# Kernel tuning notes

Hardware: AMD Instinct MI355X
Metric: run time of the kernel (lower is better)

The kernel has to match this reference:

```python
import jax, jax.numpy as jnp
import numpy as np

N_HEADS = 16
D_HEAD = 64
QUERY_DIM = 1024
CONTEXT_DIM = 1024
INNER = N_HEADS * D_HEAD


def setup_inputs() -> dict:
    key = jax.random.key(0)
    ks = jax.random.split(key, 7)
    B, Nq, Nk = 4, 1024, 1024
    x = jax.random.normal(ks[0], (B, Nq, QUERY_DIM), dtype=jnp.float32)
    context = jax.random.normal(ks[1], (B, Nk, CONTEXT_DIM), dtype=jnp.float32)
    s_q = 1.0 / np.sqrt(QUERY_DIM)
    s_c = 1.0 / np.sqrt(CONTEXT_DIM)
    s_i = 1.0 / np.sqrt(INNER)
    Wq = jax.random.uniform(ks[2], (QUERY_DIM, INNER), jnp.float32, -s_q, s_q)
    Wk = jax.random.uniform(ks[3], (CONTEXT_DIM, INNER), jnp.float32, -s_c, s_c)
    Wv = jax.random.uniform(ks[4], (CONTEXT_DIM, INNER), jnp.float32, -s_c, s_c)
    Wo = jax.random.uniform(ks[5], (INNER, QUERY_DIM), jnp.float32, -s_i, s_i)
    bo = jax.random.uniform(ks[6], (QUERY_DIM,), jnp.float32, -s_i, s_i)
    return {"x": x, "context": context, "Wq": Wq, "Wk": Wk, "Wv": Wv, "Wo": Wo, "bo": bo}


def reference(x, context, Wq, Wk, Wv, Wo, bo):
    B, Nq, _ = x.shape
    Nk = context.shape[1]
    scale = D_HEAD ** -0.5
    # project and split heads: [B, H, N, d]
    q = (x @ Wq).reshape(B, Nq, N_HEADS, D_HEAD).transpose(0, 2, 1, 3)
    k = (context @ Wk).reshape(B, Nk, N_HEADS, D_HEAD).transpose(0, 2, 1, 3)
    v = (context @ Wv).reshape(B, Nk, N_HEADS, D_HEAD).transpose(0, 2, 1, 3)
    scores = jnp.einsum("bhqd,bhkd->bhqk", q, k) * scale
    attn = jax.nn.softmax(scores, axis=-1)
    out = jnp.einsum("bhqk,bhkd->bhqd", attn, v)
    out = out.transpose(0, 2, 1, 3).reshape(B, Nq, INNER)
    return out @ Wo + bo
```

## Files before the change

### kernel.cpp

```cpp
#include <hip/hip_runtime.h>
#include <hip/hip_bf16.h>

#define BATCH 4
#define NQ 1024
#define NKK 1024
#define HD 1024
#define NHEADS 16

typedef __bf16 bf16x8 __attribute__((ext_vector_type(8)));
typedef float f32x4 __attribute__((ext_vector_type(4)));
typedef unsigned short u16;
typedef unsigned int u32;

__device__ __forceinline__ u16 f2bf(float f) {
    union { __bf16 h; u16 u; } v;
    v.h = (__bf16)f;
    return v.u;
}

#define GLOAD16(gp, lp) \
    __builtin_amdgcn_global_load_lds((const __attribute__((address_space(1))) void*)(gp), \
                                     (__attribute__((address_space(3))) void*)(lp), 16, 0, 0)

#define MFMA16(a, b, c) __builtin_amdgcn_mfma_f32_16x16x32_bf16(a, b, c, 0, 0, 0)

__global__ __launch_bounds__(256) void cvt2bf_k(const float* __restrict__ a,
                                                u16* __restrict__ o, int n4) {
    int i = blockIdx.x * blockDim.x + threadIdx.x;
    const int stride = gridDim.x * blockDim.x;
    for (; i < n4; i += stride) {
        float4 v = ((const float4*)a)[i];
        ushort4 p;
        p.x = f2bf(v.x); p.y = f2bf(v.y); p.z = f2bf(v.z); p.w = f2bf(v.w);
        ((ushort4*)o)[i] = p;
    }
}

__global__ __launch_bounds__(256) void transpose4_k(const float* __restrict__ w0,
                                                    const float* __restrict__ w1,
                                                    const float* __restrict__ w2,
                                                    const float* __restrict__ w3,
                                                    u16* __restrict__ ws) {
    const float* src = blockIdx.z == 0 ? w0 : blockIdx.z == 1 ? w1 : blockIdx.z == 2 ? w2 : w3;
    const float scl = (blockIdx.z == 0) ? 0.18033688011112042f : 1.0f;
    u16* dst = ws + (size_t)blockIdx.z * (1024u * 1024u);
    __shared__ u16 t[64][65];
    const int bx = blockIdx.x * 64;
    const int by = blockIdx.y * 64;
    const int tid = threadIdx.x;
#pragma unroll
    for (int p = 0; p < 16; ++p) {
        int idx = p * 256 + tid;
        int r = idx >> 6, c = idx & 63;
        t[c][r] = f2bf(scl * src[(size_t)(by + r) * 1024 + bx + c]);
    }
    __syncthreads();
#pragma unroll
    for (int p = 0; p < 16; ++p) {
        int idx = p * 256 + tid;
        int r = idx >> 6, c = idx & 63;
        dst[(size_t)(bx + r) * 1024 + by + c] = t[r][c];
    }
}

__global__ __launch_bounds__(512) void gemm_qkv(const u16* __restrict__ Xb,
                                                const u16* __restrict__ Cb,
                                                const u16* __restrict__ WqT,
                                                const u16* __restrict__ WkT,
                                                const u16* __restrict__ WvT,
                                                u16* __restrict__ Qb,
                                                u16* __restrict__ Kb,
                                                u16* __restrict__ VTb) {
    const int bid = blockIdx.x;
    const int swz = (bid & 7) * 96 + (bid >> 3);
    const int z = swz >> 8;
    const int rem = swz & 255;
    const int m0 = (rem >> 3) * 128;
    const int n0 = (rem & 7) * 128;

    const u16* __restrict__ A  = (z == 0) ? Xb : Cb;
    const u16* __restrict__ BT = (z == 0) ? WqT : (z == 1) ? WkT : WvT;

    __shared__ __align__(16) u16 Asm[128 * 64];
    __shared__ __align__(16) u16 Bsm[128 * 64];

    const int tid = threadIdx.x, lane = tid & 63, wv = tid >> 6;
    const int wm = wv >> 2, wn = wv & 3;
    const int lr = lane & 15, lg = lane >> 4;
    const int lx = lr & 7;
    const int M = BATCH * NQ, N = HD, K = HD;

    f32x4 acc[4][2];
#pragma unroll
    for (int i = 0; i < 4; ++i)
#pragma unroll
        for (int j = 0; j < 2; ++j) acc[i][j] = (f32x4)(0.0f);

    for (int kt = 0; kt < K; kt += 64) {
        __syncthreads();
#pragma unroll
        for (int i = 0; i < 2; ++i) {
            const int cb = (wv * 2 + i) * 64;
            const int s = cb + lane;
            const int row = s >> 3, cg = (s & 7) ^ (row & 7);
            GLOAD16(A + (size_t)(m0 + row) * K + kt + cg * 8, &Asm[cb * 8]);
            GLOAD16(BT + (size_t)(n0 + row) * K + kt + cg * 8, &Bsm[cb * 8]);
        }
        __syncthreads();
        bf16x8 af[4][2], bfr[2][2];
#pragma unroll
        for (int m = 0; m < 4; ++m)
#pragma unroll
            for (int kk = 0; kk < 2; ++kk)
                af[m][kk] = *(const bf16x8*)&Asm[((wm * 64 + m * 16 + lr) * 8 +
                                                 ((kk * 4 + lg) ^ lx)) * 8];
#pragma unroll
        for (int n = 0; n < 2; ++n)
#pragma unroll
            for (int kk = 0; kk < 2; ++kk)
                bfr[n][kk] = *(const bf16x8*)&Bsm[((wn * 32 + n * 16 + lr) * 8 +
                                                  ((kk * 4 + lg) ^ lx)) * 8];
#pragma unroll
        for (int kk = 0; kk < 2; ++kk)
#pragma unroll
            for (int m = 0; m < 4; ++m)
#pragma unroll
                for (int n = 0; n < 2; ++n)
                    acc[m][n] = MFMA16(af[m][kk], bfr[n][kk], acc[m][n]);
    }

    if (z < 2) {
        u16* __restrict__ C = (z == 0) ? Qb : Kb;
#pragma unroll
        for (int m = 0; m < 4; ++m)
#pragma unroll
            for (int n = 0; n < 2; ++n) {
                const int col = n0 + wn * 32 + n * 16 + lr;
                const int rb = m0 + wm * 64 + m * 16 + lg * 4;
#pragma unroll
                for (int r = 0; r < 4; ++r)
                    C[(size_t)(rb + r) * N + col] = f2bf(acc[m][n][r]);
            }
    } else {
#pragma unroll
        for (int m = 0; m < 4; ++m)
#pragma unroll
            for (int n = 0; n < 2; ++n) {
                const int col = n0 + wn * 32 + n * 16 + lr;
                const int rb = m0 + wm * 64 + m * 16 + lg * 4;
                ushort4 pk;
                pk.x = f2bf(acc[m][n][0]);
                pk.y = f2bf(acc[m][n][1]);
                pk.z = f2bf(acc[m][n][2]);
                pk.w = f2bf(acc[m][n][3]);
                *(ushort4*)&VTb[(size_t)col * M + rb] = pk;
            }
    }
}

__global__ __launch_bounds__(512) void gemm_out(const u16* __restrict__ A,
                                                const u16* __restrict__ BT,
                                                const float* __restrict__ bias,
                                                float* __restrict__ C) {
    const int bid = blockIdx.x;
    const int swz = (bid & 7) * 32 + (bid >> 3);
    const int m0 = (swz >> 3) * 128;
    const int n0 = (swz & 7) * 128;

    __shared__ __align__(16) u16 Asm[128 * 64];
    __shared__ __align__(16) u16 Bsm[128 * 64];

    const int tid = threadIdx.x, lane = tid & 63, wv = tid >> 6;
    const int wm = wv >> 2, wn = wv & 3;
    const int lr = lane & 15, lg = lane >> 4;
    const int lx = lr & 7;
    const int N = HD, K = HD;

    f32x4 acc[4][2];
#pragma unroll
    for (int i = 0; i < 4; ++i)
#pragma unroll
        for (int j = 0; j < 2; ++j) acc[i][j] = (f32x4)(0.0f);

    for (int kt = 0; kt < K; kt += 64) {
        __syncthreads();
#pragma unroll
        for (int i = 0; i < 2; ++i) {
            const int cb = (wv * 2 + i) * 64;
            const int s = cb + lane;
            const int row = s >> 3, cg = (s & 7) ^ (row & 7);
            GLOAD16(A + (size_t)(m0 + row) * K + kt + cg * 8, &Asm[cb * 8]);
            GLOAD16(BT + (size_t)(n0 + row) * K + kt + cg * 8, &Bsm[cb * 8]);
        }
        __syncthreads();
        bf16x8 af[4][2], bfr[2][2];
#pragma unroll
        for (int m = 0; m < 4; ++m)
#pragma unroll
            for (int kk = 0; kk < 2; ++kk)
                af[m][kk] = *(const bf16x8*)&Asm[((wm * 64 + m * 16 + lr) * 8 +
                                                 ((kk * 4 + lg) ^ lx)) * 8];
#pragma unroll
        for (int n = 0; n < 2; ++n)
#pragma unroll
            for (int kk = 0; kk < 2; ++kk)
                bfr[n][kk] = *(const bf16x8*)&Bsm[((wn * 32 + n * 16 + lr) * 8 +
                                                  ((kk * 4 + lg) ^ lx)) * 8];
#pragma unroll
        for (int kk = 0; kk < 2; ++kk)
#pragma unroll
            for (int m = 0; m < 4; ++m)
#pragma unroll
                for (int n = 0; n < 2; ++n)
                    acc[m][n] = MFMA16(af[m][kk], bfr[n][kk], acc[m][n]);
    }

#pragma unroll
    for (int m = 0; m < 4; ++m)
#pragma unroll
        for (int n = 0; n < 2; ++n) {
            const int col = n0 + wn * 32 + n * 16 + lr;
            const int rb = m0 + wm * 64 + m * 16 + lg * 4;
            const float bv = bias[col];
#pragma unroll
            for (int r = 0; r < 4; ++r)
                C[(size_t)(rb + r) * N + col] = acc[m][n][r] + bv;
        }
}

__global__ __launch_bounds__(256) void attn_k(const u16* __restrict__ Q,
                                              const u16* __restrict__ Kp,
                                              const u16* __restrict__ VT,
                                              u16* __restrict__ AO) {
    __shared__ __align__(16) u16 Ksm[2][64 * 64];
    __shared__ __align__(16) u16 Vsm[2][64 * 64];
    __shared__ __align__(16) u16 Psm[4][16 * 64];

    const int tid = threadIdx.x, lane = tid & 63, wv = tid >> 6;
    const int lr = lane & 15, lg = lane >> 4;

    const int swz = (blockIdx.x & 7) * 128 + (blockIdx.x >> 3);
    const int bh = swz >> 4;
    const int b = bh >> 4, h = bh & 15;
    const int q0 = (swz & 15) * 64 + wv * 16;
    const int lx = lr & 7;

    bf16x8 qf[2];
#pragma unroll
    for (int ks = 0; ks < 2; ++ks)
        qf[ks] = *(const bf16x8*)&Q[(size_t)(b * NQ + q0 + lr) * HD +
                                    h * 64 + ks * 32 + lg * 8];

    bf16x8 onesf;
#pragma unroll
    for (int i = 0; i < 8; ++i) onesf[i] = (__bf16)1.0f;

    const int kbase = b * NKK, vrow0 = h * 64;
    auto stageKV = [&](int kt, int bufsel) {
#pragma unroll
        for (int i = 0; i < 2; ++i) {
            const int cb = (wv * 2 + i) * 64;
            const int s = cb + lane;
            const int row = s >> 3;
            const int cg = (s & 7) ^ (row & 7);
            GLOAD16(Kp + (size_t)(kbase + kt + row) * HD + h * 64 + cg * 8,
                    &Ksm[bufsel][cb * 8]);
            GLOAD16(VT + (size_t)(vrow0 + row) * (BATCH * NKK) + kbase + kt + cg * 8,
                    &Vsm[bufsel][cb * 8]);
        }
    };

    f32x4 osum = (f32x4)(0.0f);
    f32x4 o[4];
#pragma unroll
    for (int n = 0; n < 4; ++n) o[n] = (f32x4)(0.0f);

    stageKV(0, 0);
    __syncthreads();

#pragma unroll 2
    for (int t = 0; t < NKK / 64; ++t) {
        const int cur = t & 1;
        if (t + 1 < NKK / 64) stageKV((t + 1) * 64, cur ^ 1);
        const u16* Ks = &Ksm[cur][0];
        const u16* Vs = &Vsm[cur][0];

        f32x4 s[4];
#pragma unroll
        for (int n = 0; n < 4; ++n) s[n] = (f32x4)(0.0f);
        __builtin_amdgcn_s_setprio(1);
#pragma unroll
        for (int n = 0; n < 4; ++n) {
            bf16x8 kf0 = *(const bf16x8*)&Ks[(n * 16 + lr) * 64 + (lg ^ lx) * 8];
            bf16x8 kf1 = *(const bf16x8*)&Ks[(n * 16 + lr) * 64 + ((lg | 4) ^ lx) * 8];
            s[n] = MFMA16(kf0, qf[0], s[n]);
            s[n] = MFMA16(kf1, qf[1], s[n]);
        }
        __builtin_amdgcn_s_setprio(0);

        u16* P = &Psm[wv][0];
#pragma unroll
        for (int n = 0; n < 4; ++n) {
            const float p0 = exp2f(s[n][0]);
            const float p1 = exp2f(s[n][1]);
            const float p2 = exp2f(s[n][2]);
            const float p3 = exp2f(s[n][3]);
            ushort4 pk;
            pk.x = f2bf(p0); pk.y = f2bf(p1); pk.z = f2bf(p2); pk.w = f2bf(p3);
            const int ch = (2 * n + (lg >> 1)) ^ lx;
            *(ushort4*)&P[lr * 64 + ch * 8 + (lg & 1) * 4] = pk;
        }

#pragma unroll
        for (int ks = 0; ks < 2; ++ks) {
            bf16x8 pa = *(const bf16x8*)&P[lr * 64 + (((ks * 4 + lg) ^ lx)) * 8];
            __builtin_amdgcn_s_setprio(1);
#pragma unroll
            for (int n = 0; n < 4; ++n) {
                bf16x8 vf = *(const bf16x8*)&Vs[(n * 16 + lr) * 64 + (((ks * 4 + lg) ^ lx)) * 8];
                o[n] = MFMA16(pa, vf, o[n]);
            }
            osum = MFMA16(pa, onesf, osum);
            __builtin_amdgcn_s_setprio(0);
        }
        __syncthreads();
    }

    float rs[4];
#pragma unroll
    for (int r = 0; r < 4; ++r) rs[r] = 1.0f / osum[r];

#pragma unroll
    for (int n = 0; n < 4; ++n)
#pragma unroll
        for (int r = 0; r < 4; ++r) {
            const float val = o[n][r] * rs[r];
            AO[(size_t)(b * NQ + q0 + lg * 4 + r) * HD +
               h * 64 + n * 16 + lr] = f2bf(val);
        }
}

extern "C" void kernel_launch(void* const* d_in, const int* in_sizes, int n_in,
                              void* d_out, int out_size, void* d_ws, size_t ws_size,
                              hipStream_t stream) {
    const float* x   = (const float*)d_in[0];
    const float* ctx = (const float*)d_in[1];
    const float* Wq  = (const float*)d_in[2];
    const float* Wk  = (const float*)d_in[3];
    const float* Wv  = (const float*)d_in[4];
    const float* Wo  = (const float*)d_in[5];
    const float* bo  = (const float*)d_in[6];

    u16* ws = (u16*)d_ws;
    const size_t MEG = 1024u * 1024u;
    u16* WqT = ws + 0 * MEG;
    u16* WkT = ws + 1 * MEG;
    u16* WvT = ws + 2 * MEG;
    u16* WoT = ws + 3 * MEG;
    u16* Xb  = ws + 4 * MEG;
    u16* Cb  = ws + 8 * MEG;
    u16* Qb  = ws + 12 * MEG;
    u16* Kb  = ws + 16 * MEG;
    u16* VTb = ws + 20 * MEG;
    u16* AOb = Xb;

    transpose4_k<<<dim3(16, 16, 4), 256, 0, stream>>>(Wq, Wk, Wv, Wo, ws);
    cvt2bf_k<<<4096, 256, 0, stream>>>(x,   Xb, 1024 * 1024);
    cvt2bf_k<<<4096, 256, 0, stream>>>(ctx, Cb, 1024 * 1024);
    gemm_qkv<<<768, 512, 0, stream>>>(Xb, Cb, WqT, WkT, WvT, Qb, Kb, VTb);
    attn_k<<<1024, 256, 0, stream>>>(Qb, Kb, VTb, AOb);
    gemm_out<<<256, 512, 0, stream>>>(AOb, WoT, bo, (float*)d_out);
}
```

Before: 103.1 us.

## Enlarge QKV GEMM tile to 256 rows and merge input conversion kernels

The QKV projection GEMM now uses 1024-thread blocks over 256x128 output tiles, so each B tile loaded from the concatenated transposed weights serves twice as many rows. The grid drops from 768 to 384 blocks with a new swizzle. The two fp32-to-bf16 conversion launches are merged into one kernel that covers both x and context. This trades fewer blocks and more LDS per block, with possible occupancy or tail effects, for less B-tile traffic and one fewer launch.

```diff
diff --git a/kernel.cpp b/kernel.cpp
--- a/kernel.cpp
+++ b/kernel.cpp
@@ -10,6 +10,7 @@
 typedef __bf16 bf16x8 __attribute__((ext_vector_type(8)));
 typedef float f32x4 __attribute__((ext_vector_type(4)));
 typedef unsigned short u16;
+typedef unsigned short u16x8 __attribute__((ext_vector_type(8)));
 typedef unsigned int u32;
 
 __device__ __forceinline__ u16 f2bf(float f) {
@@ -24,15 +25,21 @@
 
 #define MFMA16(a, b, c) __builtin_amdgcn_mfma_f32_16x16x32_bf16(a, b, c, 0, 0, 0)
 
-__global__ __launch_bounds__(256) void cvt2bf_k(const float* __restrict__ a,
-                                                u16* __restrict__ o, int n4) {
+__global__ __launch_bounds__(256) void cvt2bf2_k(const float* __restrict__ x,
+                                                 const float* __restrict__ ctx,
+                                                 u16* __restrict__ Xb,
+                                                 u16* __restrict__ Cb) {
+    const int half = 1024 * 1024;
     int i = blockIdx.x * blockDim.x + threadIdx.x;
     const int stride = gridDim.x * blockDim.x;
-    for (; i < n4; i += stride) {
-        float4 v = ((const float4*)a)[i];
+    for (; i < 2 * half; i += stride) {
+        const float* src = (i < half) ? x : ctx;
+        u16* dst = (i < half) ? Xb : Cb;
+        const int j = (i < half) ? i : i - half;
+        float4 v = ((const float4*)src)[j];
         ushort4 p;
         p.x = f2bf(v.x); p.y = f2bf(v.y); p.z = f2bf(v.z); p.w = f2bf(v.w);
-        ((ushort4*)o)[i] = p;
+        ((ushort4*)dst)[j] = p;
     }
 }
 
@@ -63,25 +70,23 @@
     }
 }
 
-__global__ __launch_bounds__(512) void gemm_qkv(const u16* __restrict__ Xb,
-                                                const u16* __restrict__ Cb,
-                                                const u16* __restrict__ WqT,
-                                                const u16* __restrict__ WkT,
-                                                const u16* __restrict__ WvT,
-                                                u16* __restrict__ Qb,
-                                                u16* __restrict__ Kb,
-                                                u16* __restrict__ VTb) {
+__global__ __launch_bounds__(1024) void gemm_qkv(const u16* __restrict__ Xb,
+                                                 const u16* __restrict__ Cb,
+                                                 const u16* __restrict__ BT,
+                                                 u16* __restrict__ Qb,
+                                                 u16* __restrict__ Kb,
+                                                 u16* __restrict__ VTb) {
     const int bid = blockIdx.x;
-    const int swz = (bid & 7) * 96 + (bid >> 3);
-    const int z = swz >> 8;
-    const int rem = swz & 255;
-    const int m0 = (rem >> 3) * 128;
-    const int n0 = (rem & 7) * 128;
-
-    const u16* __restrict__ A  = (z == 0) ? Xb : Cb;
-    const u16* __restrict__ BT = (z == 0) ? WqT : (z == 1) ? WkT : WvT;
-
-    __shared__ __align__(16) u16 Asm[128 * 64];
+    const int swz = (bid & 7) * 48 + (bid >> 3);
+    const int m0 = (swz / 24) * 256;
+    const int nblk = swz % 24;
+    const int n0g = nblk * 128;
+    const int z = n0g >> 10;
+    const int nc0 = n0g & 1023;
+
+    const u16* __restrict__ A = (z == 0) ? Xb : Cb;
+
+    __shared__ __align__(16) u16 Asm[256 * 64];
     __shared__ __align__(16) u16 Bsm[128 * 64];
 
     const int tid = threadIdx.x, lane = tid & 63, wv = tid >> 6;
@@ -104,7 +109,12 @@
             const int s = cb + lane;
             const int row = s >> 3, cg = (s & 7) ^ (row & 7);
             GLOAD16(A + (size_t)(m0 + row) * K + kt + cg * 8, &Asm[cb * 8]);
-            GLOAD16(BT + (size_t)(n0 + row) * K + kt + cg * 8, &Bsm[cb * 8]);
+        }
+        {
+            const int cb = wv * 64;
+            const int s = cb + lane;
+            const int row = s >> 3, cg = (s & 7) ^ (row & 7);
+            GLOAD16(BT + (size_t)(n0g + row) * K + kt + cg * 8, &Bsm[cb * 8]);
         }
         __syncthreads();
         bf16x8 af[4][2], bfr[2][2];
@@ -135,7 +145,7 @@
         for (int m = 0; m < 4; ++m)
 #pragma unroll
             for (int n = 0; n < 2; ++n) {
-                const int col = n0 + wn * 32 + n * 16 + lr;
+                const int col = nc0 + wn * 32 + n * 16 + lr;
                 const int rb = m0 + wm * 64 + m * 16 + lg * 4;
 #pragma unroll
                 for (int r = 0; r < 4; ++r)
@@ -146,7 +156,7 @@
         for (int m = 0; m < 4; ++m)
 #pragma unroll
             for (int n = 0; n < 2; ++n) {
-                const int col = n0 + wn * 32 + n * 16 + lr;
+                const int col = nc0 + wn * 32 + n * 16 + lr;
                 const int rb = m0 + wm * 64 + m * 16 + lg * 4;
                 ushort4 pk;
                 pk.x = f2bf(acc[m][n][0]);
@@ -353,9 +363,7 @@
 
     u16* ws = (u16*)d_ws;
     const size_t MEG = 1024u * 1024u;
-    u16* WqT = ws + 0 * MEG;
-    u16* WkT = ws + 1 * MEG;
-    u16* WvT = ws + 2 * MEG;
+    u16* WT3 = ws + 0 * MEG;
     u16* WoT = ws + 3 * MEG;
     u16* Xb  = ws + 4 * MEG;
     u16* Cb  = ws + 8 * MEG;
@@ -365,9 +373,8 @@
     u16* AOb = Xb;
 
     transpose4_k<<<dim3(16, 16, 4), 256, 0, stream>>>(Wq, Wk, Wv, Wo, ws);
-    cvt2bf_k<<<4096, 256, 0, stream>>>(x,   Xb, 1024 * 1024);
-    cvt2bf_k<<<4096, 256, 0, stream>>>(ctx, Cb, 1024 * 1024);
-    gemm_qkv<<<768, 512, 0, stream>>>(Xb, Cb, WqT, WkT, WvT, Qb, Kb, VTb);
+    cvt2bf2_k<<<2048, 256, 0, stream>>>(x, ctx, Xb, Cb);
+    gemm_qkv<<<384, 1024, 0, stream>>>(Xb, Cb, WT3, Qb, Kb, VTb);
     attn_k<<<1024, 256, 0, stream>>>(Qb, Kb, VTb, AOb);
     gemm_out<<<256, 512, 0, stream>>>(AOb, WoT, bo, (float*)d_out);
 }
```

New measurement: 118.7 us. 15.1% more time.
